# Performance work log

Hardware: AMD Instinct MI355X
Metric: run time of the kernel (lower is better)

Reference implementation:

```python
import jax, jax.numpy as jnp
import numpy as np

IMG, P, C = 512, 16, 1
D, DEPTH, H, DH, MLP = 768, 12, 8, 64, 2048
GRID = IMG // P          # 32
NP = GRID * GRID         # 1024 patches
N = NP + 1               # +cls token
EPS = 1e-5


def _ln(x, s, b):
    m = jnp.mean(x, -1, keepdims=True)
    v = jnp.mean((x - m) ** 2, -1, keepdims=True)
    return (x - m) * jax.lax.rsqrt(v + EPS) * s + b


def setup_inputs() -> dict:
    key = jax.random.key(0)
    ks = jax.random.split(key, 12)
    s = 0.02
    f32 = jnp.float32
    return {
        "x": jax.random.normal(ks[0], (4, C, IMG, IMG), f32),
        "conv_w": jax.random.normal(ks[1], (D, C, P, P), f32) * s,   # [out,in,kh,kw] like torch
        "conv_b": jnp.zeros((D,), f32),
        "cls_token": jax.random.normal(ks[2], (1, 1, D), f32),
        "pos_emb": jax.random.normal(ks[3], (1, N, D), f32),
        "qkv_w": jax.random.normal(ks[4], (DEPTH, D, 3 * H * DH), f32) * s,  # [in,out] layout
        "merge_w": jax.random.normal(ks[5], (DEPTH, H * DH, D), f32) * s,
        "merge_b": jnp.zeros((DEPTH, D), f32),
        "ln1_s": jnp.ones((DEPTH, D), f32),
        "ln1_b": jnp.zeros((DEPTH, D), f32),
        "ln2_s": jnp.ones((DEPTH, D), f32),
        "ln2_b": jnp.zeros((DEPTH, D), f32),
        "ffn_w1": jax.random.normal(ks[6], (DEPTH, D, MLP), f32) * s,
        "ffn_b1": jnp.zeros((DEPTH, MLP), f32),
        "ffn_w2": jax.random.normal(ks[7], (DEPTH, MLP, D), f32) * s,
        "ffn_b2": jnp.zeros((DEPTH, D), f32),
        "lnf_s": jnp.ones((D,), f32),
        "lnf_b": jnp.zeros((D,), f32),
    }


def reference(x, conv_w, conv_b, cls_token, pos_emb, qkv_w, merge_w, merge_b,
              ln1_s, ln1_b, ln2_s, ln2_b, ffn_w1, ffn_b1, ffn_w2, ffn_b2,
              lnf_s, lnf_b):
    B = x.shape[0]
    # Patch embed: stride-P conv == non-overlapping patch extraction + matmul
    xr = x.reshape(B, C, GRID, P, GRID, P)
    tok = jnp.einsum('bchpwq,dcpq->bhwd', xr, conv_w).reshape(B, NP, D) + conv_b
    t = jnp.concatenate([jnp.broadcast_to(cls_token, (B, 1, D)), tok], axis=1)
    t = t + pos_emb  # dropout is identity in eval
    scale = DH ** -0.5
    for i in range(DEPTH):
        # MSA with pre-LN
        h = _ln(t, ln1_s[i], ln1_b[i])
        qkv = (h @ qkv_w[i]).reshape(B, N, H, 3, DH)   # [B,N,H,3,DH]
        q = jnp.transpose(qkv[..., 0, :], (0, 2, 1, 3))  # [B,H,N,DH]
        k = jnp.transpose(qkv[..., 1, :], (0, 2, 1, 3))
        v = jnp.transpose(qkv[..., 2, :], (0, 2, 1, 3))
        att = jax.nn.softmax(jnp.einsum('bhnd,bhmd->bhnm', q, k) * scale, axis=-1)
        o = jnp.einsum('bhnm,bhmd->bhnd', att, v)
        o = jnp.transpose(o, (0, 2, 1, 3)).reshape(B, N, H * DH)
        t = t + (o @ merge_w[i] + merge_b[i])
        # FFN with pre-LN, exact (erf) GELU like torch nn.GELU
        h2 = _ln(t, ln2_s[i], ln2_b[i])
        f = jax.nn.gelu(h2 @ ffn_w1[i] + ffn_b1[i], approximate=False)
        t = t + (f @ ffn_w2[i] + ffn_b2[i])
    return _ln(t, lnf_s, lnf_b)
```

## Files before the change

kernel.cpp:

```cpp
#include <hip/hip_runtime.h>

#define DEV __device__ __forceinline__

typedef short s8v __attribute__((ext_vector_type(8)));
typedef float f4v __attribute__((ext_vector_type(4)));
typedef unsigned int u32x2 __attribute__((ext_vector_type(2)));

DEV short f2bf(float f) {
  unsigned u = __float_as_uint(f);
  u += 0x7FFFu + ((u >> 16) & 1u);
  return (short)(u >> 16);
}
DEV short f2bf_fast(float f) {
  return (short)((__float_as_uint(f) + 0x8000u) >> 16);
}
DEV float bf2f(short s) { return __uint_as_float(((unsigned)(unsigned short)s) << 16); }

DEV void gld_lds16(const short* g, short* l) {
  __builtin_amdgcn_global_load_lds(
      (const __attribute__((address_space(1))) void*)g,
      (__attribute__((address_space(3))) void*)l, 16, 0, 0);
}

DEV u32x2 trr(unsigned lds_byte) {
  u32x2 r;
  asm volatile("ds_read_b64_tr_b16 %0, %1" : "=&v"(r) : "v"(lds_byte));
  return r;
}

DEV int xcd_swz(int id, int nwg) {
  int q8 = nwg >> 3, r8 = nwg & 7, xcd = id & 7, off = id >> 3;
  return (xcd < r8) ? (xcd * (q8 + 1) + off) : (r8 * (q8 + 1) + (xcd - r8) * q8 + off);
}

template<int BN>
__global__ __launch_bounds__(256) void gemm_t(
    const short* __restrict__ A, const short* __restrict__ B, void* __restrict__ Cv,
    const float* __restrict__ bias,
    int M, int N, int K, int lda, int ldb, int ldc, int flags)
{
  constexpr int BPASS = BN / 32;
  constexpr int MI = (BN == 128) ? 4 : 2;
  __shared__ __align__(16) short As[2][64 * 64];
  __shared__ __align__(16) short Bs[2][BN * 64];
  int nwg = gridDim.x * gridDim.y;
  int idl = blockIdx.y * gridDim.x + blockIdx.x;
  int swz = xcd_swz(idl, nwg);
  int bx = swz % gridDim.x, by = swz / gridDim.x;
  int m0 = by * 64, n0 = bx * BN;
  int tid = threadIdx.x, lane = tid & 63, w = tid >> 6;
  int lr = lane & 15, kg = lane >> 4;
  int wrb = (BN == 128) ? 0 : (w >> 1) * 32;
  int wcb = (BN == 128) ? w * 32 : (w & 1) * 32;
  f4v acc[MI][2] = {};
  int NT = K >> 6;

#define STAGE(bufi, k0)                                                   \
  {                                                                       \
    _Pragma("unroll")                                                     \
    for (int p = 0; p < 2; ++p) {                                         \
      int ch = p * 256 + w * 64 + lane;                                   \
      int row = ch >> 3, c = (ch & 7) ^ (row & 7);                        \
      gld_lds16(A + (long)(m0 + row) * lda + (k0) + c * 8,                \
                &As[bufi][(p * 256 + w * 64) * 8]);                       \
    }                                                                     \
    _Pragma("unroll")                                                     \
    for (int p = 0; p < BPASS; ++p) {                                     \
      int ch = p * 256 + w * 64 + lane;                                   \
      int row = ch >> 3, c = (ch & 7) ^ (row & 7);                        \
      gld_lds16(B + (long)(n0 + row) * ldb + (k0) + c * 8,                \
                &Bs[bufi][(p * 256 + w * 64) * 8]);                       \
    }                                                                     \
  }

  STAGE(0, 0)
  for (int t = 0; t < NT; ++t) {
    int buf = t & 1;
    if (t + 1 < NT) {
      STAGE(buf ^ 1, (t + 1) * 64)
      if constexpr (BN == 128)
        asm volatile("s_waitcnt vmcnt(6)" ::: "memory");
      else
        asm volatile("s_waitcnt vmcnt(4)" ::: "memory");
    } else {
      asm volatile("s_waitcnt vmcnt(0)" ::: "memory");
    }
    __builtin_amdgcn_s_barrier();
    #pragma unroll
    for (int ks = 0; ks < 2; ++ks) {
      s8v av[MI], bv[2];
      #pragma unroll
      for (int mi = 0; mi < MI; ++mi) {
        int row = wrb + mi * 16 + lr;
        int sl = (ks * 4 + kg) ^ (row & 7);
        av[mi] = *(const s8v*)&As[buf][row * 64 + sl * 8];
      }
      #pragma unroll
      for (int ni = 0; ni < 2; ++ni) {
        int row = wcb + ni * 16 + lr;
        int sl = (ks * 4 + kg) ^ (row & 7);
        bv[ni] = *(const s8v*)&Bs[buf][row * 64 + sl * 8];
      }
      #pragma unroll
      for (int mi = 0; mi < MI; ++mi)
        #pragma unroll
        for (int ni = 0; ni < 2; ++ni)
          acc[mi][ni] = __builtin_amdgcn_mfma_f32_16x16x32_bf16(av[mi], bv[ni], acc[mi][ni], 0, 0, 0);
    }
    asm volatile("s_waitcnt lgkmcnt(0)" ::: "memory");
    __builtin_amdgcn_s_barrier();
  }
#undef STAGE

  float* Cf = (float*)Cv;
  short* Cb = (short*)Cv;
  #pragma unroll
  for (int mi = 0; mi < MI; ++mi)
    #pragma unroll
    for (int ni = 0; ni < 2; ++ni) {
      int col = n0 + wcb + ni * 16 + lr;
      float bvv = (flags & 1) ? bias[col] : 0.f;
      #pragma unroll
      for (int j = 0; j < 4; ++j) {
        int row = m0 + wrb + mi * 16 + kg * 4 + j;
        if (row >= M) continue;
        float v = acc[mi][ni][j] + bvv;
        if (flags & 2) v = 0.5f * v * (1.f + erff(v * 0.70710678118f));
        long ci = (long)row * ldc + col;
        if (flags & 8) Cb[ci] = f2bf(v);
        else { if (flags & 4) v += Cf[ci]; Cf[ci] = v; }
      }
    }
}

__global__ __launch_bounds__(256) void flash_k(
    const short* __restrict__ qkv, short* __restrict__ O)
{
  int swz = xcd_swz(blockIdx.x, 544);
  int z = swz / 17, qt = swz - z * 17;
  int zb = z >> 3, zh = z & 7;
  const short* base = qkv + (long)zb * 1025 * 1536 + zh * 192;
  const short* Qg = base;
  const short* Kg = base + 64;
  const short* Vg = base + 128;
  int q0 = qt * 64;
  int tid = threadIdx.x, lane = tid & 63, w = tid >> 6;
  int lr = lane & 15, kg = lane >> 4;

  __shared__ __align__(16) short Ks[2][64 * 64];
  __shared__ __align__(16) short Vs[2][64 * 64];

  s8v aq[2];
  {
    long qrow = q0 + w * 16 + lr;
    aq[0] = *(const s8v*)(Qg + qrow * 1536 + kg * 8);
    aq[1] = *(const s8v*)(Qg + qrow * 1536 + 32 + kg * 8);
  }

  unsigned vsbase = (unsigned)(unsigned long long)
      (__attribute__((address_space(3))) void*)&Vs[0][0];
  unsigned vtr = (unsigned)(lr * 8 + kg * 1024);

#define STAGE_K(bufi, kv0)                                                 \
  {                                                                        \
    int s0 = w * 128;                                                      \
    _Pragma("unroll")                                                      \
    for (int i = 0; i < 2; ++i) {                                          \
      int s = s0 + i * 64 + lane;                                          \
      int row = s >> 3, c = (s & 7) ^ (row & 7);                           \
      gld_lds16(Kg + (long)((kv0) + row) * 1536 + c * 8,                   \
                &Ks[bufi][(s0 + i * 64) * 8]);                             \
    }                                                                      \
  }
#define STAGE_V(bufi, kv0)                                                 \
  {                                                                        \
    int s0 = w * 128;                                                      \
    _Pragma("unroll")                                                      \
    for (int i = 0; i < 2; ++i) {                                          \
      int ch = s0 + i * 64 + lane;                                         \
      int st = ch >> 3, r = (ch & 7) >> 1, hh = ch & 1;                    \
      int key = (kv0) + (st >> 2) * 4 + r;                                 \
      int d = (st & 3) * 16 + hh * 8;                                      \
      gld_lds16(Vg + (long)key * 1536 + d,                                 \
                &Vs[bufi][(s0 + i * 64) * 8]);                             \
    }                                                                      \
  }

  f4v acc[4] = {};
  float m_run = -3.0e38f, l_run = 0.f;
  const float C2 = 0.18033688011112042f;

  STAGE_K(0, 0)
  STAGE_V(0, 0)
  asm volatile("s_waitcnt vmcnt(0)" ::: "memory");
  __builtin_amdgcn_s_barrier();

  for (int kt = 0; kt < 16; ++kt) {
    int cur = kt & 1;
    int kv0 = kt * 64;
    if (kt < 15) {
      STAGE_K(cur ^ 1, kv0 + 64)
      STAGE_V(cur ^ 1, kv0 + 64)
    }

    f4v sa[4] = {};
    __builtin_amdgcn_s_setprio(1);
    #pragma unroll
    for (int ni = 0; ni < 4; ++ni) {
      int row = ni * 16 + lr;
      #pragma unroll
      for (int ks = 0; ks < 2; ++ks) {
        int c = (ks * 4 + kg) ^ (row & 7);
        s8v kf = *(const s8v*)&Ks[cur][row * 64 + c * 8];
        sa[ni] = __builtin_amdgcn_mfma_f32_16x16x32_bf16(kf, aq[ks], sa[ni], 0, 0, 0);
      }
    }
    __builtin_amdgcn_s_setprio(0);

    float sv[4][4], pv[4][4];
    float tm = -3.0e38f;
    #pragma unroll
    for (int ni = 0; ni < 4; ++ni)
      #pragma unroll
      for (int jj = 0; jj < 4; ++jj) {
        float s = sa[ni][jj] * C2;
        sv[ni][jj] = s;
        tm = fmaxf(tm, s);
      }
    tm = fmaxf(tm, __shfl_xor(tm, 16));
    tm = fmaxf(tm, __shfl_xor(tm, 32));
    float m_new = fmaxf(m_run, tm);
    float scale = exp2f(m_run - m_new);
    m_run = m_new;
    float ts = 0.f;
    #pragma unroll
    for (int ni = 0; ni < 4; ++ni)
      #pragma unroll
      for (int jj = 0; jj < 4; ++jj) {
        float p = exp2f(sv[ni][jj] - m_new);
        pv[ni][jj] = p;
        ts += p;
      }
    ts += __shfl_xor(ts, 16);
    ts += __shfl_xor(ts, 32);
    l_run = l_run * scale + ts;

    float scq[4];
    #pragma unroll
    for (int jj = 0; jj < 4; ++jj)
      scq[jj] = __shfl(scale, kg * 4 + jj + 16 * kg);
    #pragma unroll
    for (int ni = 0; ni < 4; ++ni)
      #pragma unroll
      for (int jj = 0; jj < 4; ++jj) acc[ni][jj] *= scq[jj];

    unsigned pr[4][2];
    #pragma unroll
    for (int ni = 0; ni < 4; ++ni)
      #pragma unroll
      for (int h = 0; h < 2; ++h) {
        unsigned lo = (unsigned)(unsigned short)f2bf_fast(pv[ni][2 * h]);
        unsigned hi = (unsigned)(unsigned short)f2bf_fast(pv[ni][2 * h + 1]);
        pr[ni][h] = lo | (hi << 16);
      }
    union PU { s8v v; unsigned u[4]; };
    PU apu[2];
    #pragma unroll
    for (int ks = 0; ks < 2; ++ks)
      #pragma unroll
      for (int t = 0; t < 4; ++t) {
        unsigned src = (kg & 2) ? pr[2 * ks + 1][t & 1] : pr[2 * ks][t & 1];
        apu[ks].u[t] = __shfl(src, lr + 16 * (2 * (kg & 1) + (t >> 1)));
      }

    u32x2 tr[4][2][2];
    unsigned vb = vsbase + (unsigned)cur * 8192u + vtr;
    #pragma unroll
    for (int ni = 0; ni < 4; ++ni)
      #pragma unroll
      for (int ks = 0; ks < 2; ++ks) {
        tr[ni][ks][0] = trr(vb + ni * 128 + ks * 4096);
        tr[ni][ks][1] = trr(vb + ni * 128 + ks * 4096 + 512);
      }
    asm volatile("s_waitcnt lgkmcnt(0)" ::: "memory");
    __builtin_amdgcn_sched_barrier(0);

    __builtin_amdgcn_s_setprio(1);
    #pragma unroll
    for (int ni = 0; ni < 4; ++ni) {
      #pragma unroll
      for (int ks = 0; ks < 2; ++ks) {
        union { s8v v; u32x2 u2[2]; } bb;
        bb.u2[0] = tr[ni][ks][0];
        bb.u2[1] = tr[ni][ks][1];
        acc[ni] = __builtin_amdgcn_mfma_f32_16x16x32_bf16(apu[ks].v, bb.v, acc[ni], 0, 0, 0);
      }
    }
    __builtin_amdgcn_s_setprio(0);
    asm volatile("s_waitcnt lgkmcnt(0)" ::: "memory");
    asm volatile("s_waitcnt vmcnt(0)" ::: "memory");
    __builtin_amdgcn_s_barrier();
  }
#undef STAGE_K
#undef STAGE_V

  {
    s8v k0 = *(const s8v*)(Kg + 1024L * 1536 + kg * 8);
    s8v k1 = *(const s8v*)(Kg + 1024L * 1536 + 32 + kg * 8);
    float s = 0.f;
    #pragma unroll
    for (int j = 0; j < 8; ++j)
      s += bf2f(aq[0][j]) * bf2f(k0[j]) + bf2f(aq[1][j]) * bf2f(k1[j]);
    s += __shfl_xor(s, 16);
    s += __shfl_xor(s, 32);
    float sC = s * C2;
    float m_new = fmaxf(m_run, sC);
    float sc = exp2f(m_run - m_new);
    float p = exp2f(sC - m_new);
    l_run = l_run * sc + p;
    float vrow[4];
    #pragma unroll
    for (int ni = 0; ni < 4; ++ni)
      vrow[ni] = bf2f(Vg[1024L * 1536 + ni * 16 + lr]);
    float scq[4], pq[4];
    #pragma unroll
    for (int jj = 0; jj < 4; ++jj) {
      scq[jj] = __shfl(sc, kg * 4 + jj + 16 * kg);
      pq[jj]  = __shfl(p,  kg * 4 + jj + 16 * kg);
    }
    #pragma unroll
    for (int ni = 0; ni < 4; ++ni)
      #pragma unroll
      for (int jj = 0; jj < 4; ++jj)
        acc[ni][jj] = acc[ni][jj] * scq[jj] + pq[jj] * vrow[ni];
  }

  float linv = 1.f / l_run;
  float invq[4];
  #pragma unroll
  for (int jj = 0; jj < 4; ++jj)
    invq[jj] = __shfl(linv, kg * 4 + jj + 16 * kg);
  #pragma unroll
  for (int ni = 0; ni < 4; ++ni)
    #pragma unroll
    for (int jj = 0; jj < 4; ++jj) {
      int row = q0 + w * 16 + kg * 4 + jj;
      if (row < 1025)
        O[((long)(zb * 1025 + row)) * 512 + zh * 64 + ni * 16 + lr] = f2bf(acc[ni][jj] * invq[jj]);
    }
}

DEV void tconv_body(const float* w, short* wt, int K, int N, int bx, int by, int tid)
{
  __shared__ float tile[32][33];
  int n0 = bx * 32, k0 = by * 32;
  int tx = tid & 31, ty = tid >> 5;
  #pragma unroll
  for (int j = 0; j < 4; ++j)
    tile[ty + j * 8][tx] = w[(long)(k0 + ty + j * 8) * N + n0 + tx];
  __syncthreads();
  #pragma unroll
  for (int j = 0; j < 4; ++j)
    wt[(long)(n0 + ty + j * 8) * K + k0 + tx] = f2bf(tile[tx][ty + j * 8]);
}

__global__ __launch_bounds__(256) void tconv4_k(
    const float* __restrict__ sq, const float* __restrict__ sm,
    const float* __restrict__ sf1, const float* __restrict__ sf2,
    short* __restrict__ dq, short* __restrict__ dm,
    short* __restrict__ df1, short* __restrict__ df2)
{
  int id = blockIdx.x, tid = threadIdx.x;
  if (id < 1152)       tconv_body(sq,  dq,  768, 1536, id % 48,          id / 48,          tid);
  else if (id < 1536)  tconv_body(sm,  dm,  512, 768,  (id - 1152) % 24, (id - 1152) / 24, tid);
  else if (id < 3072)  tconv_body(sf1, df1, 768, 2048, (id - 1536) % 64, (id - 1536) / 64, tid);
  else                 tconv_body(sf2, df2, 2048, 768, (id - 3072) % 24, (id - 3072) / 24, tid);
}

__global__ __launch_bounds__(256) void cvt_k(const float* __restrict__ in,
    short* __restrict__ out, int n)
{
  int i = blockIdx.x * 256 + threadIdx.x;
  if (i < n) out[i] = f2bf(in[i]);
}

DEV void st_ln(float* p, float v) { *p = v; }
DEV void st_ln(short* p, float v) { *p = f2bf(v); }

template<typename OT>
__global__ __launch_bounds__(256) void ln_k(const float* __restrict__ x,
    const float* __restrict__ g, const float* __restrict__ b,
    OT* __restrict__ y, int rows)
{
  int row = blockIdx.x;
  if (row >= rows) return;
  const float* xr = x + (long)row * 768;
  OT* yr = y + (long)row * 768;
  int t = threadIdx.x;
  float v0 = xr[t], v1 = xr[t + 256], v2 = xr[t + 512];
  float s = v0 + v1 + v2, s2 = v0 * v0 + v1 * v1 + v2 * v2;
  #pragma unroll
  for (int o = 32; o > 0; o >>= 1) { s += __shfl_down(s, o); s2 += __shfl_down(s2, o); }
  __shared__ float as_[4], as2_[4];
  if ((t & 63) == 0) { as_[t >> 6] = s; as2_[t >> 6] = s2; }
  __syncthreads();
  s = as_[0] + as_[1] + as_[2] + as_[3];
  s2 = as2_[0] + as2_[1] + as2_[2] + as2_[3];
  float mean = s * (1.f / 768.f);
  float var = s2 * (1.f / 768.f) - mean * mean;
  float r = rsqrtf(var + 1e-5f);
  st_ln(&yr[t],       (v0 - mean) * r * g[t]       + b[t]);
  st_ln(&yr[t + 256], (v1 - mean) * r * g[t + 256] + b[t + 256]);
  st_ln(&yr[t + 512], (v2 - mean) * r * g[t + 512] + b[t + 512]);
}

__global__ __launch_bounds__(256) void im2col_k(const float* __restrict__ x,
    short* __restrict__ A)
{
  int i = blockIdx.x * 256 + threadIdx.x;
  int k = i & 255, row = i >> 8;
  int px = k & 15, py = k >> 4;
  int gx = row & 31, gy = (row >> 5) & 31, b = row >> 10;
  A[i] = f2bf(x[((long)(b * 512) + gy * 16 + py) * 512 + gx * 16 + px]);
}

__global__ __launch_bounds__(256) void assemble_k(const short* __restrict__ tok,
    const float* __restrict__ cls, const float* __restrict__ pos, float* __restrict__ t)
{
  int i = blockIdx.x * 256 + threadIdx.x;
  int d = i % 768; int rn = i / 768; int n = rn % 1025; int b = rn / 1025;
  float v = (n == 0) ? cls[d] : bf2f(tok[((long)(b * 1024 + n - 1)) * 768 + d]);
  t[i] = v + pos[n * 768 + d];
}

extern "C" void kernel_launch(void* const* d_in, const int* in_sizes, int n_in,
                              void* d_out, int out_size, void* d_ws, size_t ws_size,
                              hipStream_t stream)
{
  const float* x       = (const float*)d_in[0];
  const float* conv_w  = (const float*)d_in[1];
  const float* conv_b  = (const float*)d_in[2];
  const float* cls     = (const float*)d_in[3];
  const float* pos     = (const float*)d_in[4];
  const float* qkv_w   = (const float*)d_in[5];
  const float* merge_w = (const float*)d_in[6];
  const float* merge_b = (const float*)d_in[7];
  const float* ln1_s   = (const float*)d_in[8];
  const float* ln1_b   = (const float*)d_in[9];
  const float* ln2_s   = (const float*)d_in[10];
  const float* ln2_b   = (const float*)d_in[11];
  const float* ffn_w1  = (const float*)d_in[12];
  const float* ffn_b1  = (const float*)d_in[13];
  const float* ffn_w2  = (const float*)d_in[14];
  const float* ffn_b2  = (const float*)d_in[15];
  const float* lnf_s   = (const float*)d_in[16];
  const float* lnf_b   = (const float*)d_in[17];

  char* wsp = (char*)d_ws;
  size_t o = 0;
  auto take = [&](size_t bytes) { char* r = wsp + o; o = (o + bytes + 255) & ~(size_t)255; return r; };
  short* wq   = (short*)take(1536ul * 768 * 2);
  short* wm   = (short*)take(768ul * 512 * 2);
  short* wf1  = (short*)take(2048ul * 768 * 2);
  short* wf2  = (short*)take(768ul * 2048 * 2);
  short* wcv  = (short*)take(768ul * 256 * 2);
  float* t    = (float*)take(4100ul * 768 * 4);
  char*  hO   = take(4352ul * 768 * 2);
  short* qkv  = (short*)take(4ul * 1025 * 1536 * 2);
  char*  fV   = take(4352ul * 2048 * 2);
  take(2ul << 20);

  short* h   = (short*)hO;
  short* O   = (short*)hO;
  short* f   = (short*)fV;
  short* imc = (short*)fV;
  short* tok = (short*)(fV + 4096ul * 256 * 2);

  dim3 blk(256);

  cvt_k<<<768, blk, 0, stream>>>(conv_w, wcv, 768 * 256);
  im2col_k<<<4096, blk, 0, stream>>>(x, imc);
  gemm_t<64><<<dim3(12, 64), blk, 0, stream>>>(imc, wcv, tok, conv_b,
      4096, 768, 256, 256, 256, 768, 1 | 8);
  assemble_k<<<12300, blk, 0, stream>>>(tok, cls, pos, t);

  for (int i = 0; i < 12; ++i) {
    tconv4_k<<<4608, blk, 0, stream>>>(
        qkv_w + (long)i * 768 * 1536, merge_w + (long)i * 512 * 768,
        ffn_w1 + (long)i * 768 * 2048, ffn_w2 + (long)i * 2048 * 768,
        wq, wm, wf1, wf2);

    ln_k<short><<<4100, blk, 0, stream>>>(t, ln1_s + i * 768, ln1_b + i * 768, h, 4100);
    gemm_t<128><<<dim3(12, 65), blk, 0, stream>>>(h, wq, qkv, nullptr,
        4100, 1536, 768, 768, 768, 1536, 8);
    flash_k<<<544, blk, 0, stream>>>(qkv, O);
    gemm_t<64><<<dim3(12, 65), blk, 0, stream>>>(O, wm, t, merge_b + i * 768,
        4100, 768, 512, 512, 512, 768, 1 | 4);
    ln_k<short><<<4100, blk, 0, stream>>>(t, ln2_s + i * 768, ln2_b + i * 768, h, 4100);
    gemm_t<128><<<dim3(16, 65), blk, 0, stream>>>(h, wf1, f, ffn_b1 + i * 2048,
        4100, 2048, 768, 768, 768, 2048, 1 | 2 | 8);
    gemm_t<64><<<dim3(12, 65), blk, 0, stream>>>(f, wf2, t, ffn_b2 + i * 768,
        4100, 768, 2048, 2048, 2048, 768, 1 | 4);
  }
  ln_k<float><<<4100, blk, 0, stream>>>(t, lnf_s, lnf_b, (float*)d_out, 4100);
}
```

Before: 2.096 ms.

## Split attention KV range across two blocks with combine kernel, lazy rescale

```diff
diff --git a/kernel.cpp b/kernel.cpp
--- a/kernel.cpp
+++ b/kernel.cpp
@@ -134,16 +134,18 @@
 }
 
 __global__ __launch_bounds__(256) void flash_k(
-    const short* __restrict__ qkv, short* __restrict__ O)
-{
-  int swz = xcd_swz(blockIdx.x, 544);
-  int z = swz / 17, qt = swz - z * 17;
+    const short* __restrict__ qkv, float* __restrict__ Opart, float* __restrict__ ML)
+{
+  int swz = xcd_swz(blockIdx.x, 1088);
+  int h = swz / 544, rem = swz - h * 544;
+  int z = rem / 17, qt = rem - z * 17;
   int zb = z >> 3, zh = z & 7;
   const short* base = qkv + (long)zb * 1025 * 1536 + zh * 192;
   const short* Qg = base;
   const short* Kg = base + 64;
   const short* Vg = base + 128;
   int q0 = qt * 64;
+  int kt0 = h * 8;
   int tid = threadIdx.x, lane = tid & 63, w = tid >> 6;
   int lr = lane & 15, kg = lane >> 4;
 
@@ -189,18 +191,18 @@
   f4v acc[4] = {};
   float m_run = -3.0e38f, l_run = 0.f;
   const float C2 = 0.18033688011112042f;
-
-  STAGE_K(0, 0)
-  STAGE_V(0, 0)
+  const float THR = 44.36f;
+
+  STAGE_K(0, kt0 * 64)
+  STAGE_V(0, kt0 * 64)
   asm volatile("s_waitcnt vmcnt(0)" ::: "memory");
   __builtin_amdgcn_s_barrier();
 
-  for (int kt = 0; kt < 16; ++kt) {
-    int cur = kt & 1;
-    int kv0 = kt * 64;
-    if (kt < 15) {
-      STAGE_K(cur ^ 1, kv0 + 64)
-      STAGE_V(cur ^ 1, kv0 + 64)
+  for (int kt = kt0; kt < kt0 + 8; ++kt) {
+    int cur = (kt - kt0) & 1;
+    if (kt + 1 < kt0 + 8) {
+      STAGE_K(cur ^ 1, (kt + 1) * 64)
+      STAGE_V(cur ^ 1, (kt + 1) * 64)
     }
 
     f4v sa[4] = {};
@@ -217,51 +219,53 @@
     }
     __builtin_amdgcn_s_setprio(0);
 
-    float sv[4][4], pv[4][4];
     float tm = -3.0e38f;
     #pragma unroll
     for (int ni = 0; ni < 4; ++ni)
       #pragma unroll
-      for (int jj = 0; jj < 4; ++jj) {
-        float s = sa[ni][jj] * C2;
-        sv[ni][jj] = s;
-        tm = fmaxf(tm, s);
-      }
+      for (int jj = 0; jj < 4; ++jj) tm = fmaxf(tm, sa[ni][jj]);
     tm = fmaxf(tm, __shfl_xor(tm, 16));
     tm = fmaxf(tm, __shfl_xor(tm, 32));
-    float m_new = fmaxf(m_run, tm);
-    float scale = exp2f(m_run - m_new);
-    m_run = m_new;
+    bool need = !__all(tm <= m_run + THR);
+    float scale = 1.f;
+    if (need) {
+      float m_new = fmaxf(m_run, tm);
+      scale = exp2f((m_run - m_new) * C2);
+      m_run = m_new;
+    }
+    float mC = m_run * C2;
+    float pv[4][4];
     float ts = 0.f;
     #pragma unroll
     for (int ni = 0; ni < 4; ++ni)
       #pragma unroll
       for (int jj = 0; jj < 4; ++jj) {
-        float p = exp2f(sv[ni][jj] - m_new);
+        float p = exp2f(fmaf(sa[ni][jj], C2, -mC));
         pv[ni][jj] = p;
         ts += p;
       }
     ts += __shfl_xor(ts, 16);
     ts += __shfl_xor(ts, 32);
     l_run = l_run * scale + ts;
-
-    float scq[4];
-    #pragma unroll
-    for (int jj = 0; jj < 4; ++jj)
-      scq[jj] = __shfl(scale, kg * 4 + jj + 16 * kg);
+    if (need) {
+      float scq[4];
+      #pragma unroll
+      for (int jj = 0; jj < 4; ++jj)
+        scq[jj] = __shfl(scale, kg * 4 + jj + 16 * kg);
+      #pragma unroll
+      for (int ni = 0; ni < 4; ++ni)
+        #pragma unroll
+        for (int jj = 0; jj < 4; ++jj) acc[ni][jj] *= scq[jj];
+    }
+
+    unsigned pr[4][2];
     #pragma unroll
     for (int ni = 0; ni < 4; ++ni)
       #pragma unroll
-      for (int jj = 0; jj < 4; ++jj) acc[ni][jj] *= scq[jj];
-
-    unsigned pr[4][2];
-    #pragma unroll
-    for (int ni = 0; ni < 4; ++ni)
-      #pragma unroll
-      for (int h = 0; h < 2; ++h) {
-        unsigned lo = (unsigned)(unsigned short)f2bf_fast(pv[ni][2 * h]);
-        unsigned hi = (unsigned)(unsigned short)f2bf_fast(pv[ni][2 * h + 1]);
-        pr[ni][h] = lo | (hi << 16);
+      for (int hh = 0; hh < 2; ++hh) {
+        unsigned lo = (unsigned)(unsigned short)f2bf_fast(pv[ni][2 * hh]);
+        unsigned hi = (unsigned)(unsigned short)f2bf_fast(pv[ni][2 * hh + 1]);
+        pr[ni][hh] = lo | (hi << 16);
       }
     union PU { s8v v; unsigned u[4]; };
     PU apu[2];
@@ -304,7 +308,7 @@
 #undef STAGE_K
 #undef STAGE_V
 
-  {
+  if (h) {
     s8v k0 = *(const s8v*)(Kg + 1024L * 1536 + kg * 8);
     s8v k1 = *(const s8v*)(Kg + 1024L * 1536 + 32 + kg * 8);
     float s = 0.f;
@@ -313,10 +317,10 @@
       s += bf2f(aq[0][j]) * bf2f(k0[j]) + bf2f(aq[1][j]) * bf2f(k1[j]);
     s += __shfl_xor(s, 16);
     s += __shfl_xor(s, 32);
-    float sC = s * C2;
-    float m_new = fmaxf(m_run, sC);
-    float sc = exp2f(m_run - m_new);
-    float p = exp2f(sC - m_new);
+    float m_new = fmaxf(m_run, s);
+    float sc = exp2f((m_run - m_new) * C2);
+    float p = exp2f((s - m_new) * C2);
+    m_run = m_new;
     l_run = l_run * sc + p;
     float vrow[4];
     #pragma unroll
@@ -335,19 +339,39 @@
         acc[ni][jj] = acc[ni][jj] * scq[jj] + pq[jj] * vrow[ni];
   }
 
-  float linv = 1.f / l_run;
-  float invq[4];
-  #pragma unroll
-  for (int jj = 0; jj < 4; ++jj)
-    invq[jj] = __shfl(linv, kg * 4 + jj + 16 * kg);
+  long zrow = (long)(h * 32 + z) * 1025;
+  if (kg == 0) {
+    int row = q0 + w * 16 + lr;
+    if (row < 1025) {
+      ML[(zrow + row) * 2]     = m_run * C2;
+      ML[(zrow + row) * 2 + 1] = l_run;
+    }
+  }
   #pragma unroll
   for (int ni = 0; ni < 4; ++ni)
     #pragma unroll
     for (int jj = 0; jj < 4; ++jj) {
       int row = q0 + w * 16 + kg * 4 + jj;
       if (row < 1025)
-        O[((long)(zb * 1025 + row)) * 512 + zh * 64 + ni * 16 + lr] = f2bf(acc[ni][jj] * invq[jj]);
-    }
+        Opart[(zrow + row) * 64 + ni * 16 + lr] = acc[ni][jj];
+    }
+}
+
+__global__ __launch_bounds__(256) void fcomb_k(
+    const float* __restrict__ Opart, const float* __restrict__ ML, short* __restrict__ O)
+{
+  int idx = blockIdx.x * 256 + threadIdx.x;
+  int d = idx & 63;
+  int r = idx >> 6;
+  int z = r / 1025, row = r - z * 1025;
+  float m0 = ML[(long)r * 2], l0 = ML[(long)r * 2 + 1];
+  float m1 = ML[(long)(32800 + r) * 2], l1 = ML[(long)(32800 + r) * 2 + 1];
+  float M = fmaxf(m0, m1);
+  float w0 = exp2f(m0 - M), w1 = exp2f(m1 - M);
+  float inv = 1.f / (l0 * w0 + l1 * w1);
+  float v = (Opart[(long)r * 64 + d] * w0 + Opart[(long)(32800 + r) * 64 + d] * w1) * inv;
+  int zb = z >> 3, zh = z & 7;
+  O[((long)(zb * 1025 + row)) * 512 + zh * 64 + d] = f2bf(v);
 }
 
 DEV void tconv_body(const float* w, short* wt, int K, int N, int bx, int by, int tid)
@@ -470,11 +494,13 @@
   char*  fV   = take(4352ul * 2048 * 2);
   take(2ul << 20);
 
-  short* h   = (short*)hO;
-  short* O   = (short*)hO;
-  short* f   = (short*)fV;
-  short* imc = (short*)fV;
-  short* tok = (short*)(fV + 4096ul * 256 * 2);
+  short* h     = (short*)hO;
+  short* O     = (short*)hO;
+  short* f     = (short*)fV;
+  short* imc   = (short*)fV;
+  short* tok   = (short*)(fV + 4096ul * 256 * 2);
+  float* Opart = (float*)fV;
+  float* ML    = (float*)(fV + 16793600);
 
   dim3 blk(256);
 
@@ -491,13 +517,14 @@
         wq, wm, wf1, wf2);
 
     ln_k<short><<<4100, blk, 0, stream>>>(t, ln1_s + i * 768, ln1_b + i * 768, h, 4100);
-    gemm_t<128><<<dim3(12, 65), blk, 0, stream>>>(h, wq, qkv, nullptr,
+    gemm_t<64><<<dim3(24, 65), blk, 0, stream>>>(h, wq, qkv, nullptr,
         4100, 1536, 768, 768, 768, 1536, 8);
-    flash_k<<<544, blk, 0, stream>>>(qkv, O);
+    flash_k<<<1088, blk, 0, stream>>>(qkv, Opart, ML);
+    fcomb_k<<<8200, blk, 0, stream>>>(Opart, ML, O);
     gemm_t<64><<<dim3(12, 65), blk, 0, stream>>>(O, wm, t, merge_b + i * 768,
         4100, 768, 512, 512, 512, 768, 1 | 4);
     ln_k<short><<<4100, blk, 0, stream>>>(t, ln2_s + i * 768, ln2_b + i * 768, h, 4100);
-    gemm_t<128><<<dim3(16, 65), blk, 0, stream>>>(h, wf1, f, ffn_b1 + i * 2048,
+    gemm_t<64><<<dim3(32, 65), blk, 0, stream>>>(h, wf1, f, ffn_b1 + i * 2048,
         4100, 2048, 768, 768, 768, 2048, 1 | 2 | 8);
     gemm_t<64><<<dim3(12, 65), blk, 0, stream>>>(f, wf2, t, ffn_b2 + i * 768,
         4100, 768, 2048, 2048, 2048, 768, 1 | 4);
```

New measurement: 2.034 ms. -3.0%, faster.
